# Kernel optimization log

Hardware: AMD Instinct MI355X
Metric: run time of the kernel (lower is better)

Reference implementation:

```python
import jax, jax.numpy as jnp
import numpy as np

N, E = 50000, 800000
DIN, DH, DOUT = 128, 64, 16


def setup_inputs() -> dict:
    key = jax.random.key(0)
    ks = jax.random.split(key, 8)
    s = lambda d: np.float32(1.0 / np.sqrt(d))
    return {
        "x": jax.random.normal(ks[0], (N, DIN), jnp.float32),
        "edge_index": jax.random.randint(ks[1], (2, E), 0, N, dtype=jnp.int32),
        "w0": jax.random.normal(ks[2], (DIN, DH), jnp.float32) * s(DIN),
        "b0": jnp.zeros((DH,), jnp.float32),
        "w1": jax.random.normal(ks[3], (DH, DH), jnp.float32) * s(DH),
        "b1": jnp.zeros((DH,), jnp.float32),
        "w2": jax.random.normal(ks[4], (DH, DH), jnp.float32) * s(DH),
        "b2": jnp.zeros((DH,), jnp.float32),
        "fc_w": jax.random.normal(ks[5], (DH, DOUT), jnp.float32) * s(DH),
        "fc_b": jnp.zeros((DOUT,), jnp.float32),
    }


def reference(x, edge_index, w0, b0, w1, b1, w2, b2, fc_w, fc_b):
    n = x.shape[0]
    loop = jnp.arange(n, dtype=edge_index.dtype)
    # PyG GCNConv default: add self-loops, symmetric normalization
    src = jnp.concatenate([edge_index[0], loop])  # [E+N]
    dst = jnp.concatenate([edge_index[1], loop])
    deg = jax.ops.segment_sum(jnp.ones_like(dst, dtype=x.dtype), dst, num_segments=n)
    dinv = jnp.where(deg > 0, jax.lax.rsqrt(deg), 0.0)
    norm = dinv[src] * dinv[dst]  # [E+N]

    def conv(h, W, b):
        h = h @ W                            # [N, DH]
        msg = h[src] * norm[:, None]         # [E+N, DH] gather + scale
        return jax.ops.segment_sum(msg, dst, num_segments=n) + b

    h = jax.nn.elu(conv(x, w0, b0))
    h = jax.nn.elu(conv(h, w1, b1))
    h = jax.nn.elu(conv(h, w2, b2))
    return jax.nn.softmax(h @ fc_w + fc_b, axis=1)
```

## Files before the change

kernel.cpp:

```cpp
#include <hip/hip_runtime.h>
#include <hip/hip_fp16.h>
#include <math.h>

#define DIN 128
#define DH  64
#define DOUT 16
#define NWIN 8

__global__ __launch_bounds__(256) void deg_kernel(const int* __restrict__ dst,
                                                  int* __restrict__ counts, int E) {
    int e = blockIdx.x * 256 + threadIdx.x;
    if (e < E) atomicAdd(&counts[dst[e]], 1);
}

__global__ __launch_bounds__(256) void alloc_kernel(const int* __restrict__ counts,
                                                    int* __restrict__ gtotal,
                                                    int* __restrict__ offs,
                                                    int* __restrict__ cursor,
                                                    float* __restrict__ dinv, int n) {
    int i = blockIdx.x * 256 + threadIdx.x;
    if (i >= n) return;
    int c = counts[i];
    int pad = (c + 7) & ~7;
    int o = atomicAdd(gtotal, pad);
    offs[i] = o;
    cursor[i] = o;
    dinv[i] = rsqrtf((float)(c + 1));
}

__global__ __launch_bounds__(256) void fill_kernel(int* __restrict__ a, int v, int cap) {
    int i = blockIdx.x * 256 + threadIdx.x;
    if (i < cap) a[i] = v;
}

__global__ __launch_bounds__(256) void scatter_kernel(const int* __restrict__ src,
                                                      const int* __restrict__ dst,
                                                      int* __restrict__ cursor,
                                                      int* __restrict__ csr_src,
                                                      int E, int winSize) {
    int win = blockIdx.x & (NWIN - 1);
    int group = blockIdx.x >> 3;
    int nGroups = gridDim.x >> 3;
    int lo = win * winSize, hi = lo + winSize;
    int stride = nGroups * 256;
    for (int e = group * 256 + threadIdx.x; e < E; e += stride) {
        int d = dst[e];
        if (d >= lo && d < hi) {
            int j = atomicAdd(&cursor[d], 1);
            csr_src[j] = src[e];
        }
    }
}

__global__ __launch_bounds__(256) void mm128_kernel(const float* __restrict__ H,
                                                    const float* __restrict__ W,
                                                    const float* __restrict__ dinv,
                                                    __half* __restrict__ T, int n) {
    __shared__ __align__(16) float wl[128 * 64];
    __shared__ __align__(16) float hl[128][36];
    int tid = threadIdx.x;
    int row0 = blockIdx.x * 32;
    for (int i = tid; i < 128 * 64; i += 256) wl[i] = W[i];
    for (int i = tid; i < 32 * 128; i += 256) {
        int r = i >> 7, k = i & 127;
        int rr = row0 + r;
        hl[k][r] = (rr < n) ? H[(size_t)rr * 128 + k] : 0.f;
    }
    if (blockIdx.x == 0 && tid < 64) T[(size_t)n * 64 + tid] = __float2half(0.f);
    __syncthreads();
    int col = tid & 63;
    int w8 = (tid >> 6) * 8;
    float a0=0,a1=0,a2=0,a3=0,a4=0,a5=0,a6=0,a7=0;
    #pragma unroll 4
    for (int k = 0; k < 128; ++k) {
        float wv = wl[k * 64 + col];
        float4 h4a = *reinterpret_cast<const float4*>(&hl[k][w8]);
        float4 h4b = *reinterpret_cast<const float4*>(&hl[k][w8 + 4]);
        a0 += h4a.x * wv; a1 += h4a.y * wv; a2 += h4a.z * wv; a3 += h4a.w * wv;
        a4 += h4b.x * wv; a5 += h4b.y * wv; a6 += h4b.z * wv; a7 += h4b.w * wv;
    }
    int r0 = row0 + w8;
    float acc[8] = {a0,a1,a2,a3,a4,a5,a6,a7};
    #pragma unroll
    for (int r = 0; r < 8; ++r)
        if (r0 + r < n) T[(size_t)(r0 + r) * 64 + col] = __float2half(acc[r] * dinv[r0 + r]);
}

__global__ __launch_bounds__(256) void aggmm_kernel(const __half* __restrict__ T,
                                                    const int* __restrict__ offs,
                                                    const int* __restrict__ cnt,
                                                    const int* __restrict__ csr_src,
                                                    const float* __restrict__ dinv,
                                                    const float* __restrict__ bias,
                                                    const float* __restrict__ Wn,
                                                    __half* __restrict__ out, int n) {
    __shared__ __align__(16) float wl[64 * 64];
    __shared__ __align__(16) float rowbuf[8][68];
    int tid = threadIdx.x;
    for (int i = tid; i < 64 * 64; i += 256) wl[i] = Wn[i];
    if (blockIdx.x == 0 && tid < 64) out[(size_t)n * 64 + tid] = __float2half(0.f);
    __syncthreads();
    int hw = tid >> 5;
    int f2 = tid & 31;
    int node = blockIdx.x * 8 + hw;
    if (node >= n) return;

    const __half2* T2 = reinterpret_cast<const __half2*>(T);
    float di = dinv[node];
    int e0 = offs[node];
    int e1 = e0 + ((cnt[node] + 7) & ~7);
    float2 sv = __half22float2(T2[(size_t)node * 32 + f2]);
    float ax0 = sv.x, ay0 = sv.y;
    float ax1=0, ay1=0, ax2=0, ay2=0, ax3=0, ay3=0;
    #pragma unroll 1
    for (int e = e0; e < e1; e += 8) {
        int4 sa = *reinterpret_cast<const int4*>(&csr_src[e]);
        int4 sb = *reinterpret_cast<const int4*>(&csr_src[e + 4]);
        float2 v0 = __half22float2(T2[(size_t)sa.x * 32 + f2]);
        float2 v1 = __half22float2(T2[(size_t)sa.y * 32 + f2]);
        float2 v2 = __half22float2(T2[(size_t)sa.z * 32 + f2]);
        float2 v3 = __half22float2(T2[(size_t)sa.w * 32 + f2]);
        float2 v4 = __half22float2(T2[(size_t)sb.x * 32 + f2]);
        float2 v5 = __half22float2(T2[(size_t)sb.y * 32 + f2]);
        float2 v6 = __half22float2(T2[(size_t)sb.z * 32 + f2]);
        float2 v7 = __half22float2(T2[(size_t)sb.w * 32 + f2]);
        ax0 += v0.x + v4.x;  ay0 += v0.y + v4.y;
        ax1 += v1.x + v5.x;  ay1 += v1.y + v5.y;
        ax2 += v2.x + v6.x;  ay2 += v2.y + v6.y;
        ax3 += v3.x + v7.x;  ay3 += v3.y + v7.y;
    }
    float hx = (ax0 + ax1) + (ax2 + ax3);
    float hy = (ay0 + ay1) + (ay2 + ay3);
    float2 bv = *reinterpret_cast<const float2*>(&bias[2 * f2]);
    hx = hx * di + bv.x;
    hy = hy * di + bv.y;
    hx = hx > 0.f ? hx : expm1f(hx);
    hy = hy > 0.f ? hy : expm1f(hy);

    *reinterpret_cast<float2*>(&rowbuf[hw][2 * f2]) = make_float2(hx, hy);
    float ox = 0.f, oy = 0.f;
    #pragma unroll
    for (int k0 = 0; k0 < 64; k0 += 4) {
        float4 r4 = *reinterpret_cast<const float4*>(&rowbuf[hw][k0]);
        float2 w0 = *reinterpret_cast<const float2*>(&wl[(k0 + 0) * 64 + 2 * f2]);
        float2 w1 = *reinterpret_cast<const float2*>(&wl[(k0 + 1) * 64 + 2 * f2]);
        float2 w2 = *reinterpret_cast<const float2*>(&wl[(k0 + 2) * 64 + 2 * f2]);
        float2 w3 = *reinterpret_cast<const float2*>(&wl[(k0 + 3) * 64 + 2 * f2]);
        ox = fmaf(r4.x, w0.x, ox); oy = fmaf(r4.x, w0.y, oy);
        ox = fmaf(r4.y, w1.x, ox); oy = fmaf(r4.y, w1.y, oy);
        ox = fmaf(r4.z, w2.x, ox); oy = fmaf(r4.z, w2.y, oy);
        ox = fmaf(r4.w, w3.x, ox); oy = fmaf(r4.w, w3.y, oy);
    }
    __half2* out2 = reinterpret_cast<__half2*>(out);
    out2[(size_t)node * 32 + f2] = __float22half2_rn(make_float2(ox * di, oy * di));
}

__global__ __launch_bounds__(256) void aggfc_kernel(const __half* __restrict__ T,
                                                    const int* __restrict__ offs,
                                                    const int* __restrict__ cnt,
                                                    const int* __restrict__ csr_src,
                                                    const float* __restrict__ dinv,
                                                    const float* __restrict__ bias,
                                                    const float* __restrict__ fcw,
                                                    const float* __restrict__ fcb,
                                                    float* __restrict__ out, int n) {
    __shared__ __align__(16) float wl[64 * 17];
    __shared__ __align__(16) float rowbuf[8][68];
    int tid = threadIdx.x;
    for (int i = tid; i < 64 * 16; i += 256) {
        int k = i >> 4, j = i & 15;
        wl[k * 17 + j] = fcw[i];
    }
    __syncthreads();
    int hw = tid >> 5, f2 = tid & 31;
    int node = blockIdx.x * 8 + hw;
    if (node >= n) return;

    const __half2* T2 = reinterpret_cast<const __half2*>(T);
    float di = dinv[node];
    int e0 = offs[node];
    int e1 = e0 + ((cnt[node] + 7) & ~7);
    float2 sv = __half22float2(T2[(size_t)node * 32 + f2]);
    float ax0 = sv.x, ay0 = sv.y;
    float ax1=0, ay1=0, ax2=0, ay2=0, ax3=0, ay3=0;
    #pragma unroll 1
    for (int e = e0; e < e1; e += 8) {
        int4 sa = *reinterpret_cast<const int4*>(&csr_src[e]);
        int4 sb = *reinterpret_cast<const int4*>(&csr_src[e + 4]);
        float2 v0 = __half22float2(T2[(size_t)sa.x * 32 + f2]);
        float2 v1 = __half22float2(T2[(size_t)sa.y * 32 + f2]);
        float2 v2 = __half22float2(T2[(size_t)sa.z * 32 + f2]);
        float2 v3 = __half22float2(T2[(size_t)sa.w * 32 + f2]);
        float2 v4 = __half22float2(T2[(size_t)sb.x * 32 + f2]);
        float2 v5 = __half22float2(T2[(size_t)sb.y * 32 + f2]);
        float2 v6 = __half22float2(T2[(size_t)sb.z * 32 + f2]);
        float2 v7 = __half22float2(T2[(size_t)sb.w * 32 + f2]);
        ax0 += v0.x + v4.x;  ay0 += v0.y + v4.y;
        ax1 += v1.x + v5.x;  ay1 += v1.y + v5.y;
        ax2 += v2.x + v6.x;  ay2 += v2.y + v6.y;
        ax3 += v3.x + v7.x;  ay3 += v3.y + v7.y;
    }
    float hx = (ax0 + ax1) + (ax2 + ax3);
    float hy = (ay0 + ay1) + (ay2 + ay3);
    float2 bv = *reinterpret_cast<const float2*>(&bias[2 * f2]);
    hx = hx * di + bv.x;
    hy = hy * di + bv.y;
    hx = hx > 0.f ? hx : expm1f(hx);
    hy = hy > 0.f ? hy : expm1f(hy);
    *reinterpret_cast<float2*>(&rowbuf[hw][2 * f2]) = make_float2(hx, hy);

    int g = f2 >> 4;
    int j = f2 & 15;
    float o = 0.f;
    #pragma unroll
    for (int kk = 0; kk < 32; ++kk) {
        int k = g * 32 + kk;
        o += rowbuf[hw][k] * wl[k * 17 + j];
    }
    o += __shfl_xor(o, 16, 64);
    o += fcb[j];
    float m = o;
    #pragma unroll
    for (int d = 8; d; d >>= 1) m = fmaxf(m, __shfl_xor(m, d, 64));
    float ex = expf(o - m);
    float s = ex;
    #pragma unroll
    for (int d = 8; d; d >>= 1) s += __shfl_xor(s, d, 64);
    if ((f2 & 16) == 0) out[(size_t)node * 16 + j] = ex / s;
}

extern "C" void kernel_launch(void* const* d_in, const int* in_sizes, int n_in,
                              void* d_out, int out_size, void* d_ws, size_t ws_size,
                              hipStream_t stream) {
    const float* x   = (const float*)d_in[0];
    const int*   ei  = (const int*)d_in[1];
    const float* w0  = (const float*)d_in[2];
    const float* b0  = (const float*)d_in[3];
    const float* w1  = (const float*)d_in[4];
    const float* b1  = (const float*)d_in[5];
    const float* w2  = (const float*)d_in[6];
    const float* b2  = (const float*)d_in[7];
    const float* fcw = (const float*)d_in[8];
    const float* fcb = (const float*)d_in[9];
    float* out = (float*)d_out;

    const int N = in_sizes[0] / DIN;
    const int E = in_sizes[1] / 2;
    const int* src = ei;
    const int* dst = ei + E;
    const int csr_cap = E + 8 * N + 8;

    char* p = (char*)d_ws;
    auto take = [&](size_t bytes) {
        char* q = p;
        p += (bytes + 255) & ~(size_t)255;
        return q;
    };
    int*    counts  = (int*)take((size_t)(N + 1) * 4);
    int*    gtotal  = counts + N;
    int*    offs    = (int*)take((size_t)N * 4);
    int*    cursor  = (int*)take((size_t)N * 4);
    float*  dinv    = (float*)take((size_t)N * 4);
    int*    csr_src = (int*)take((size_t)csr_cap * 4);
    __half* tbufA   = (__half*)take((size_t)(N + 1) * DH * 2);
    __half* tbufB   = (__half*)take((size_t)(N + 1) * DH * 2);

    hipMemsetAsync(counts, 0, (size_t)(N + 1) * 4, stream);

    deg_kernel<<<(E + 255) / 256, 256, 0, stream>>>(dst, counts, E);
    alloc_kernel<<<(N + 255) / 256, 256, 0, stream>>>(counts, gtotal, offs, cursor, dinv, N);
    fill_kernel<<<(csr_cap + 255) / 256, 256, 0, stream>>>(csr_src, N, csr_cap);
    int winSize = (N + NWIN - 1) / NWIN;
    scatter_kernel<<<1024, 256, 0, stream>>>(src, dst, cursor, csr_src, E, winSize);

    int node_grid = (N + 7) / 8;

    mm128_kernel<<<(N + 31) / 32, 256, 0, stream>>>(x, w0, dinv, tbufA, N);
    aggmm_kernel<<<node_grid, 256, 0, stream>>>(tbufA, offs, counts, csr_src,
                                                dinv, b0, w1, tbufB, N);
    aggmm_kernel<<<node_grid, 256, 0, stream>>>(tbufB, offs, counts, csr_src,
                                                dinv, b1, w2, tbufA, N);
    aggfc_kernel<<<node_grid, 256, 0, stream>>>(tbufA, offs, counts, csr_src,
                                                dinv, b2, fcw, fcb, out, N);
}
```

Before: 301.0 us.

## Use split-fp16 MFMA for the first-layer 128x64 matmul

```diff
diff --git a/kernel.cpp b/kernel.cpp
--- a/kernel.cpp
+++ b/kernel.cpp
@@ -6,6 +6,9 @@
 #define DH  64
 #define DOUT 16
 #define NWIN 8
+
+typedef _Float16 f16x8 __attribute__((ext_vector_type(8)));
+typedef float f32x4 __attribute__((ext_vector_type(4)));
 
 __global__ __launch_bounds__(256) void deg_kernel(const int* __restrict__ dst,
                                                   int* __restrict__ counts, int E) {
@@ -52,38 +55,78 @@
     }
 }
 
-__global__ __launch_bounds__(256) void mm128_kernel(const float* __restrict__ H,
-                                                    const float* __restrict__ W,
-                                                    const float* __restrict__ dinv,
-                                                    __half* __restrict__ T, int n) {
-    __shared__ __align__(16) float wl[128 * 64];
-    __shared__ __align__(16) float hl[128][36];
+__global__ __launch_bounds__(256) void mm128_mfma(const float* __restrict__ H,
+                                                  const float* __restrict__ W,
+                                                  const float* __restrict__ dinv,
+                                                  __half* __restrict__ T, int n, int nTiles) {
+    __shared__ _Float16 bhi[4][4][64][8];
+    __shared__ _Float16 blo[4][4][64][8];
     int tid = threadIdx.x;
-    int row0 = blockIdx.x * 32;
-    for (int i = tid; i < 128 * 64; i += 256) wl[i] = W[i];
-    for (int i = tid; i < 32 * 128; i += 256) {
-        int r = i >> 7, k = i & 127;
-        int rr = row0 + r;
-        hl[k][r] = (rr < n) ? H[(size_t)rr * 128 + k] : 0.f;
+    for (int it = 0; it < 32; ++it) {
+        int idx = it * 256 + tid;
+        int k = idx >> 6, nn = idx & 63;
+        float w = W[idx];
+        _Float16 h = (_Float16)w;
+        _Float16 l = (_Float16)(w - (float)h);
+        int kt = k >> 5, kr = k & 31;
+        int g = kr >> 3, j = kr & 7;
+        int ct = nn >> 4, c = nn & 15;
+        int ln = g * 16 + c;
+        bhi[kt][ct][ln][j] = h;
+        blo[kt][ct][ln][j] = l;
     }
     if (blockIdx.x == 0 && tid < 64) T[(size_t)n * 64 + tid] = __float2half(0.f);
     __syncthreads();
-    int col = tid & 63;
-    int w8 = (tid >> 6) * 8;
-    float a0=0,a1=0,a2=0,a3=0,a4=0,a5=0,a6=0,a7=0;
-    #pragma unroll 4
-    for (int k = 0; k < 128; ++k) {
-        float wv = wl[k * 64 + col];
-        float4 h4a = *reinterpret_cast<const float4*>(&hl[k][w8]);
-        float4 h4b = *reinterpret_cast<const float4*>(&hl[k][w8 + 4]);
-        a0 += h4a.x * wv; a1 += h4a.y * wv; a2 += h4a.z * wv; a3 += h4a.w * wv;
-        a4 += h4b.x * wv; a5 += h4b.y * wv; a6 += h4b.z * wv; a7 += h4b.w * wv;
-    }
-    int r0 = row0 + w8;
-    float acc[8] = {a0,a1,a2,a3,a4,a5,a6,a7};
-    #pragma unroll
-    for (int r = 0; r < 8; ++r)
-        if (r0 + r < n) T[(size_t)(r0 + r) * 64 + col] = __float2half(acc[r] * dinv[r0 + r]);
+
+    int wave = blockIdx.x * 4 + (tid >> 6);
+    if (wave >= nTiles) return;
+    int lane = tid & 63;
+    f16x8 Bh[4][4], Bl[4][4];
+    #pragma unroll
+    for (int kt = 0; kt < 4; ++kt)
+        #pragma unroll
+        for (int ct = 0; ct < 4; ++ct) {
+            Bh[kt][ct] = *(const f16x8*)&bhi[kt][ct][lane][0];
+            Bl[kt][ct] = *(const f16x8*)&blo[kt][ct][lane][0];
+        }
+    int row0 = wave * 16;
+    int arow = row0 + (lane & 15);
+    if (arow >= n) arow = n - 1;
+    const float* hp = H + (size_t)arow * 128 + ((lane >> 4) << 3);
+    f32x4 acc[4];
+    #pragma unroll
+    for (int ct = 0; ct < 4; ++ct) acc[ct] = (f32x4){0.f, 0.f, 0.f, 0.f};
+    #pragma unroll
+    for (int kt = 0; kt < 4; ++kt) {
+        float4 p0 = *(const float4*)(hp + kt * 32);
+        float4 p1 = *(const float4*)(hp + kt * 32 + 4);
+        float v[8] = {p0.x, p0.y, p0.z, p0.w, p1.x, p1.y, p1.z, p1.w};
+        f16x8 ah, al;
+        #pragma unroll
+        for (int j = 0; j < 8; ++j) {
+            _Float16 h = (_Float16)v[j];
+            ah[j] = h;
+            al[j] = (_Float16)(v[j] - (float)h);
+        }
+        #pragma unroll
+        for (int ct = 0; ct < 4; ++ct) {
+            acc[ct] = __builtin_amdgcn_mfma_f32_16x16x32_f16(ah, Bh[kt][ct], acc[ct], 0, 0, 0);
+            acc[ct] = __builtin_amdgcn_mfma_f32_16x16x32_f16(al, Bh[kt][ct], acc[ct], 0, 0, 0);
+            acc[ct] = __builtin_amdgcn_mfma_f32_16x16x32_f16(ah, Bl[kt][ct], acc[ct], 0, 0, 0);
+        }
+    }
+    int rbase = row0 + ((lane >> 4) << 2);
+    int cbase = lane & 15;
+    #pragma unroll
+    for (int r = 0; r < 4; ++r) {
+        int row = rbase + r;
+        if (row < n) {
+            float d = dinv[row];
+            #pragma unroll
+            for (int ct = 0; ct < 4; ++ct)
+                T[(size_t)row * 64 + ct * 16 + cbase] = __float2half(acc[ct][r] * d);
+        }
+    }
 }
 
 __global__ __launch_bounds__(256) void aggmm_kernel(const __half* __restrict__ T,
@@ -274,8 +317,9 @@
     scatter_kernel<<<1024, 256, 0, stream>>>(src, dst, cursor, csr_src, E, winSize);
 
     int node_grid = (N + 7) / 8;
-
-    mm128_kernel<<<(N + 31) / 32, 256, 0, stream>>>(x, w0, dinv, tbufA, N);
+    int nTiles = (N + 15) / 16;
+
+    mm128_mfma<<<(nTiles + 3) / 4, 256, 0, stream>>>(x, w0, dinv, tbufA, N, nTiles);
     aggmm_kernel<<<node_grid, 256, 0, stream>>>(tbufA, offs, counts, csr_src,
                                                 dinv, b0, w1, tbufB, N);
     aggmm_kernel<<<node_grid, 256, 0, stream>>>(tbufB, offs, counts, csr_src,
```

Result: faster. 278.2 us (-7.6%).
